# Kernel optimization log

Measured on AMD Instinct MI355X. Metric: run time of the kernel, lower is better.

Reference implementation:

```python
import jax, jax.numpy as jnp
import numpy as np

B, T, M, D = 2, 2048, 2048, 128
H = M // D
ROTARY_BASE = 10000
NORM_EPS = 1e-6
QK_SCALE = 1.0 / D  # mult = sqrt(qk_scale) applied to both q and k
INFTY_APPROX = 1e30


def setup_inputs() -> dict:
    key = jax.random.key(0)
    ks = jax.random.split(key, 6)
    w_scale = M ** (-0.5)
    return {
        "x": jax.random.normal(ks[0], (B, T, M), jnp.float32),
        "wq": jax.random.normal(ks[1], (M, H, D), jnp.float32) * w_scale,
        "wk": jax.random.normal(ks[2], (M, H, D), jnp.float32) * w_scale,
        "wv": jax.random.normal(ks[3], (M, H, D), jnp.float32) * w_scale,
        "wo": jax.random.normal(ks[4], (H, D, M), jnp.float32) * w_scale,
        "gq": jnp.zeros((H, 1, D), jnp.float32),
        "bq": jnp.zeros((H, 1, D), jnp.float32),
        "gk": jnp.zeros((H, 1, D), jnp.float32),
        "bk": jnp.zeros((H, 1, D), jnp.float32),
    }


def _qk_layernorm(x, g, b):
    # x: [B,H,T,D]; g,b: [H,1,D]; centered RMS norm with trainable (1+g), b
    x = x - jnp.mean(x, axis=-1, keepdims=True)
    x = x / jnp.sqrt(jnp.mean(jnp.square(x), axis=-1, keepdims=True) + NORM_EPS)
    return x * (1.0 + g)[None] + b[None]


def _rotary(x):
    # x: [B,H,T,D]; half-split rotary encoding
    half = D // 2
    positions = jnp.arange(T, dtype=jnp.float32)[:, None]          # [T,1]
    ang_freqs = jnp.power(float(ROTARY_BASE), -jnp.arange(half, dtype=jnp.float32) / half)[None, :]  # [1,half]
    radians = positions * ang_freqs                                  # [T,half]
    cos = jnp.cos(radians)[None, None].astype(x.dtype)               # [1,1,T,half]
    sin = jnp.sin(radians)[None, None].astype(x.dtype)
    even, odd = jnp.split(x, 2, axis=-1)
    return jnp.concatenate([even * cos - odd * sin, even * sin + odd * cos], axis=-1)


def reference(x, wq, wk, wv, wo, gq, bq, gk, bk):
    q = jnp.einsum('bim,mhd->bhid', x, wq)
    k = jnp.einsum('bim,mhd->bhid', x, wk)
    v = jnp.einsum('bim,mhd->bhid', x, wv)
    q = _rotary(_qk_layernorm(q, gq, bq))
    k = _rotary(_qk_layernorm(k, gk, bk))
    mult = jnp.asarray(QK_SCALE ** 0.5, dtype=x.dtype)
    s = jnp.einsum('bhid,bhjd->bhij', q * mult, k * mult)            # [B,H,T,T]
    i = jnp.arange(T)[:, None]
    j = jnp.arange(T)[None, :]
    future = (i < j)[None, None]                                      # mask future positions
    s = s - jnp.asarray(INFTY_APPROX, dtype=s.dtype) * future
    p = jax.nn.softmax(s, axis=-1)
    o = jnp.einsum('bhij,bhjd->bhid', p, v)
    return jnp.einsum('bhid,hdm->bim', o, wo)
```

## Files before the change

kernel.cpp:

```cpp
#include <hip/hip_runtime.h>


#define NB 2
#define NT 2048
#define NM 2048
#define NH 16
#define ND 128

typedef __attribute__((ext_vector_type(4))) float f32x4;
typedef __attribute__((ext_vector_type(8))) short bf16x8;
typedef __attribute__((ext_vector_type(4))) short bf16x4;

#define AS1 __attribute__((address_space(1)))
#define AS3 __attribute__((address_space(3)))

#define SW(r) (((r) ^ ((r) >> 2)) & 3)

__device__ __forceinline__ unsigned short f2bf(float f){
  unsigned int u = __float_as_uint(f);
  u = (u + 0x7fffu + ((u >> 16) & 1u)) >> 16;
  return (unsigned short)u;
}
__device__ __forceinline__ float bf2f(short s){
  return __uint_as_float(((unsigned int)(unsigned short)s) << 16);
}
__device__ __forceinline__ void gload_lds16(const void* g, void* l){
  __builtin_amdgcn_global_load_lds((const AS1 void*)g, (AS3 void*)l, 16, 0, 0);
}

__global__ __launch_bounds__(256) void prep_k(const float* __restrict__ x,
                                              const float* __restrict__ wq,
                                              const float* __restrict__ wk,
                                              const float* __restrict__ wv,
                                              const float* __restrict__ wo,
                                              short* __restrict__ xb,
                                              short* __restrict__ wT,
                                              float* __restrict__ ctab,
                                              float* __restrict__ stab){
  __shared__ float tl[32][33];
  const int bid = blockIdx.x, tid = threadIdx.x;
  if (bid < 8192){
    size_t gid = (size_t)bid * 256 + tid;
    float4 v = *(const float4*)(x + gid * 4);
    bf16x4 o;
    o[0] = (short)f2bf(v.x); o[1] = (short)f2bf(v.y);
    o[2] = (short)f2bf(v.z); o[3] = (short)f2bf(v.w);
    *(bf16x4*)(xb + gid * 4) = o;
  } else if (bid < 24576){
    int tb = bid - 8192;
    int z = tb >> 12, rem = tb & 4095;
    int n0 = (rem & 63) * 32, k0 = (rem >> 6) * 32;
    const float* src = (z == 0) ? wq : (z == 1) ? wk : (z == 2) ? wv : wo;
    short* dst = wT + (size_t)z * 2048 * 2048;
    int cx = tid & 31, ry = tid >> 5;
    #pragma unroll
    for (int p = 0; p < 4; ++p)
      tl[ry + 8 * p][cx] = src[(size_t)(k0 + ry + 8 * p) * 2048 + n0 + cx];
    __syncthreads();
    #pragma unroll
    for (int p = 0; p < 4; ++p){
      int n = n0 + ry + 8 * p;
      if (z < 2){
        int d = n & 127;
        n = (n & ~127) | (((d & 63) << 1) | (d >> 6));
      }
      dst[(size_t)n * 2048 + k0 + cx] = (short)f2bf(tl[cx][ry + 8 * p]);
    }
  } else {
    int t = (bid - 24576) * 4 + (tid >> 6);
    int i = tid & 63;
    float freq = __expf(-(float)i * (9.210340371976184f / 64.0f));
    float ang = (float)t * freq;
    ctab[t * 64 + i] = cosf(ang);
    stab[t * 64 + i] = sinf(ang);
  }
}

#define NKT2 64
__global__ __launch_bounds__(512, 4) void gemm256_k(const short* __restrict__ A,
                                                    const short* __restrict__ Bt,
                                                    short* __restrict__ Cv,
                                                    short* __restrict__ Cn,
                                                    const float* __restrict__ gq,
                                                    const float* __restrict__ bq,
                                                    const float* __restrict__ gk,
                                                    const float* __restrict__ bk,
                                                    const float* __restrict__ ctab,
                                                    const float* __restrict__ stab){
  extern __shared__ char lds[];
  const int tid = threadIdx.x;
  const int wid = tid >> 6, lane = tid & 63;
  const int lrow = lane & 15, g8 = lane >> 4;
  const int wm = wid >> 1, wn = wid & 1;
  const int Kdim = 2048;

  int bid = blockIdx.x;
  int s = (bid & 7) * 96 + (bid >> 3);
  const int bx = s & 15;
  const int by = s >> 4;
  const int m0 = bx * 256, n0 = by * 128;

  const int ar = lane >> 2;
  const int ag = (lane & 3) ^ SW(ar);
  const short* Ab = A  + (size_t)(m0 + wid * 32 + ar) * Kdim + ag * 8;
  const short* Bb = Bt + (size_t)(n0 + wid * 16 + ar) * Kdim + ag * 8;

  f32x4 acc[4][4] = {};

  auto STAGE = [&](int c, int kt){
    #pragma unroll
    for (int i = 0; i < 2; ++i)
      gload_lds16(Ab + (size_t)(i * 16) * Kdim + kt * 32,
                  lds + c * 16384 + wid * 2048 + i * 1024);
    gload_lds16(Bb + kt * 32, lds + 32768 + c * 8192 + wid * 1024);
  };
  auto ldA = [&](int c, int mi) -> bf16x8 {
    int row = wm * 64 + mi * 16 + lrow;
    return *(const bf16x8*)(lds + c * 16384 + row * 64 + ((g8 ^ SW(row)) << 4));
  };
  auto ldB = [&](int c, int ni) -> bf16x8 {
    int row = wn * 64 + ni * 16 + lrow;
    return *(const bf16x8*)(lds + 32768 + c * 8192 + row * 64 + ((g8 ^ SW(row)) << 4));
  };

  STAGE(0, 0);

  for (int kt = 0; kt < NKT2; ++kt){
    const int c = kt & 1;
    asm volatile("s_waitcnt vmcnt(0)" ::: "memory");
    __builtin_amdgcn_s_barrier();
    if (kt + 1 < NKT2) STAGE(c ^ 1, kt + 1);

    bf16x8 af[4], bfv[4];
    #pragma unroll
    for (int mi = 0; mi < 4; ++mi) af[mi] = ldA(c, mi);
    #pragma unroll
    for (int ni = 0; ni < 4; ++ni) bfv[ni] = ldB(c, ni);
    #pragma unroll
    for (int mi = 0; mi < 4; ++mi)
      #pragma unroll
      for (int ni = 0; ni < 4; ++ni)
        acc[mi][ni] = __builtin_amdgcn_mfma_f32_16x16x32_bf16(
            af[mi], bfv[ni], acc[mi][ni], 0, 0, 0);
  }

  const int tsel = by >> 4;
  const int hh = by & 15;
  if (tsel < 2){
    const float* gv = tsel ? gk : gq;
    const float* bv = tsel ? bk : bq;
    float* red = (float*)lds;
    float gcoef[4], bcoef[4];
    #pragma unroll
    for (int ni = 0; ni < 4; ++ni){
      int p = wn * 64 + ni * 16 + lrow;
      int d = (p >> 1) + ((p & 1) << 6);
      gcoef[ni] = 1.0f + gv[hh * 128 + d];
      bcoef[ni] = bv[hh * 128 + d];
    }
    __syncthreads();
    #pragma unroll
    for (int mi = 0; mi < 4; ++mi)
      #pragma unroll
      for (int r = 0; r < 4; ++r){
        float a0 = acc[mi][0][r], a1 = acc[mi][1][r];
        float a2 = acc[mi][2][r], a3 = acc[mi][3][r];
        float s1 = (a0 + a1) + (a2 + a3);
        float s2 = (a0*a0 + a1*a1) + (a2*a2 + a3*a3);
        #pragma unroll
        for (int off = 1; off < 16; off <<= 1){
          s1 += __shfl_xor(s1, off);
          s2 += __shfl_xor(s2, off);
        }
        if (lrow == 0){
          int row = wm * 64 + mi * 16 + g8 * 4 + r;
          red[row * 4 + wn * 2]     = s1;
          red[row * 4 + wn * 2 + 1] = s2;
        }
      }
    __syncthreads();
    const float qsc = tsel ? 1.0f : 0.011271055007f;
    const float sgn = (lrow & 1) ? 1.0f : -1.0f;
    short* dstn = Cn + (size_t)tsel * (NB * NH * NT * ND);
    #pragma unroll
    for (int mi = 0; mi < 4; ++mi)
      #pragma unroll
      for (int r = 0; r < 4; ++r){
        int row = wm * 64 + mi * 16 + g8 * 4 + r;
        float s1 = red[row * 4] + red[row * 4 + 2];
        float s2 = red[row * 4 + 1] + red[row * 4 + 3];
        float mean = s1 * (1.0f / 128.0f);
        float var = s2 * (1.0f / 128.0f) - mean * mean;
        float rstd = rsqrtf(var + 1e-6f);
        int rowb = m0 + row;
        int b = rowb >> 11, t = rowb & 2047;
        size_t rbase = (((size_t)(b * NH + hh)) * NT + t) * ND;
        #pragma unroll
        for (int ni = 0; ni < 4; ++ni){
          float nv = (acc[mi][ni][r] - mean) * rstd * gcoef[ni] + bcoef[ni];
          float pv = __shfl_xor(nv, 1);
          int p = wn * 64 + ni * 16 + lrow;
          float c = ctab[t * 64 + (p >> 1)], sn = stab[t * 64 + (p >> 1)];
          float o = (nv * c + sgn * pv * sn) * qsc;
          dstn[rbase + p] = (short)f2bf(o);
        }
      }
  } else {
    #pragma unroll
    for (int mi = 0; mi < 4; ++mi){
      int rowb = m0 + wm * 64 + mi * 16 + g8 * 4;
      int b = rowb >> 11, t0 = rowb & 2047;
      int jb = t0 >> 6, toff = t0 & 63;
      #pragma unroll
      for (int ni = 0; ni < 4; ++ni){
        int d = wn * 64 + ni * 16 + lrow;
        f32x4 a = acc[mi][ni];
        bf16x4 w4;
        #pragma unroll
        for (int r = 0; r < 4; ++r) w4[r] = (short)f2bf(a[r]);
        *(bf16x4*)&Cv[(((size_t)(b * NH + hh) * 32 + jb) * ND + d) * 64 + toff] = w4;
      }
    }
  }
}

__global__ __launch_bounds__(512, 4) void gemmo_k(const short* __restrict__ A,
                                                  const short* __restrict__ Bt,
                                                  float* __restrict__ Cout){
  extern __shared__ char lds[];
  const int tid = threadIdx.x;
  const int wid = tid >> 6, lane = tid & 63;
  const int lrow = lane & 15, g8 = lane >> 4;
  const int wm = wid >> 1, wn = wid & 1;
  const int Kdim = 2048;

  int bid = blockIdx.x;
  int s = (bid & 7) * 32 + (bid >> 3);
  const int bx = s & 15;
  const int by = s >> 4;
  const int m0 = bx * 256, n0 = by * 128;

  const int ar = lane >> 2;
  const int ag = (lane & 3) ^ SW(ar);
  const short* Ab = A  + (size_t)(m0 + wid * 32 + ar) * Kdim + ag * 8;
  const short* Bb = Bt + (size_t)(n0 + wid * 16 + ar) * Kdim + ag * 8;

  f32x4 acc[4][4] = {};

  auto STAGE = [&](int c, int kt){
    #pragma unroll
    for (int i = 0; i < 2; ++i)
      gload_lds16(Ab + (size_t)(i * 16) * Kdim + kt * 32,
                  lds + c * 16384 + wid * 2048 + i * 1024);
    gload_lds16(Bb + kt * 32, lds + 32768 + c * 8192 + wid * 1024);
  };
  auto ldA = [&](int c, int mi) -> bf16x8 {
    int row = wm * 64 + mi * 16 + lrow;
    return *(const bf16x8*)(lds + c * 16384 + row * 64 + ((g8 ^ SW(row)) << 4));
  };
  auto ldB = [&](int c, int ni) -> bf16x8 {
    int row = wn * 64 + ni * 16 + lrow;
    return *(const bf16x8*)(lds + 32768 + c * 8192 + row * 64 + ((g8 ^ SW(row)) << 4));
  };

  STAGE(0, 0);

  for (int kt = 0; kt < NKT2; ++kt){
    const int c = kt & 1;
    asm volatile("s_waitcnt vmcnt(0)" ::: "memory");
    __builtin_amdgcn_s_barrier();
    if (kt + 1 < NKT2) STAGE(c ^ 1, kt + 1);

    bf16x8 af[4], bfv[4];
    #pragma unroll
    for (int mi = 0; mi < 4; ++mi) af[mi] = ldA(c, mi);
    #pragma unroll
    for (int ni = 0; ni < 4; ++ni) bfv[ni] = ldB(c, ni);
    #pragma unroll
    for (int mi = 0; mi < 4; ++mi)
      #pragma unroll
      for (int ni = 0; ni < 4; ++ni)
        acc[mi][ni] = __builtin_amdgcn_mfma_f32_16x16x32_bf16(
            af[mi], bfv[ni], acc[mi][ni], 0, 0, 0);
  }

  #pragma unroll
  for (int mi = 0; mi < 4; ++mi){
    int rowb = m0 + wm * 64 + mi * 16 + g8 * 4;
    #pragma unroll
    for (int ni = 0; ni < 4; ++ni){
      int col = n0 + wn * 64 + ni * 16 + lrow;
      f32x4 a = acc[mi][ni];
      #pragma unroll
      for (int r = 0; r < 4; ++r)
        Cout[(size_t)(rowb + r) * 2048 + col] = a[r];
    }
  }
}

__global__ __launch_bounds__(512) void attn_k(const short* __restrict__ qn,
                                              const short* __restrict__ kn,
                                              const short* __restrict__ vt,
                                              short* __restrict__ ob){
  extern __shared__ char lds[];
  const int tid = threadIdx.x;
  const int wid = tid >> 6, lane = tid & 63;
  const int lrow = lane & 15, g8 = lane >> 4;
  const int id = blockIdx.x;
  const int qs = id >> 5;
  const int bh = id & 31;
  const int b = bh >> 4, h = bh & 15;
  const size_t base = (size_t)bh * NT * ND;
  char* Pw = lds + 98304 + wid * 2048;

  auto STAGE = [&](int jb){
    const int cb = jb % 3;
    #pragma unroll
    for (int i = 0; i < 2; ++i){
      int r0 = wid * 4 + i * 32;
      int r = r0 + (lane >> 4);
      int g = lane & 15;
      gload_lds16(kn + base + (size_t)(jb * 64 + r) * ND + ((g ^ (r & 7)) << 3),
                  lds + cb * 16384 + r0 * 256);
    }
    #pragma unroll
    for (int i = 0; i < 2; ++i){
      int d0 = wid * 8 + i * 64;
      int d = d0 + (lane >> 3);
      int g = lane & 7;
      gload_lds16(vt + base + (size_t)jb * 8192 + d * 64 + ((g ^ (d & 7)) << 3),
                  lds + 49152 + cb * 16384 + d0 * 128);
    }
  };

  for (int pass = 0; pass < 2; ++pass){
    const int qt = pass ? (15 - qs) : qs;
    const int t0 = qt * 128;
    const int wrow0 = t0 + wid * 16;
    const int tq = wrow0 + lrow;
    bf16x8 qf[4];
    #pragma unroll
    for (int dc = 0; dc < 4; ++dc)
      qf[dc] = *(const bf16x8*)(qn + base + (size_t)tq * ND + dc * 32 + g8 * 8);
    f32x4 O[8] = {};
    float m = -3e38f, lsum = 0.0f;
    const int ntiles = 2 * qt + 2;

    __syncthreads();
    STAGE(0);
    STAGE(1);

    for (int jb = 0; jb < ntiles; ++jb){
      if (jb + 1 < ntiles) asm volatile("s_waitcnt vmcnt(4)" ::: "memory");
      else                 asm volatile("s_waitcnt vmcnt(0)" ::: "memory");
      __builtin_amdgcn_s_barrier();
      if (jb + 2 < ntiles) STAGE(jb + 2);
      const char* Kb = lds + (jb % 3) * 16384;
      const char* Vb = lds + 49152 + (jb % 3) * 16384;

      if (jb * 64 <= wrow0 + 15){
        f32x4 st[4] = {};
        __builtin_amdgcn_s_setprio(1);
        #pragma unroll
        for (int dc = 0; dc < 4; ++dc)
          #pragma unroll
          for (int js = 0; js < 4; ++js){
            int jl = js * 16 + lrow;
            bf16x8 kf = *(const bf16x8*)(Kb + jl * 256 +
                          (((dc * 4 + g8) ^ (jl & 7)) << 4));
            st[js] = __builtin_amdgcn_mfma_f32_16x16x32_bf16(kf, qf[dc], st[js], 0, 0, 0);
          }
        __builtin_amdgcn_s_setprio(0);
        if (jb * 64 + 63 > wrow0){
          #pragma unroll
          for (int js = 0; js < 4; ++js)
            #pragma unroll
            for (int r = 0; r < 4; ++r){
              int j = jb * 64 + js * 16 + g8 * 4 + r;
              if (j > tq) st[js][r] = -3e38f;
            }
        }
        f32x4 m4 = st[0];
        #pragma unroll
        for (int js = 1; js < 4; ++js)
          #pragma unroll
          for (int r = 0; r < 4; ++r) m4[r] = fmaxf(m4[r], st[js][r]);
        float mx = fmaxf(fmaxf(m4[0], m4[1]), fmaxf(m4[2], m4[3]));
        mx = fmaxf(mx, __shfl_xor(mx, 16));
        mx = fmaxf(mx, __shfl_xor(mx, 32));
        if (!__all(mx <= m + 8.0f)){
          float mnew = fmaxf(m, mx);
          float fac = exp2f(m - mnew);
          m = mnew;
          lsum *= fac;
          #pragma unroll
          for (int dcb = 0; dcb < 8; ++dcb) O[dcb] *= fac;
        }
        float ps = 0.0f;
        #pragma unroll
        for (int js = 0; js < 4; ++js){
          float p0 = exp2f(st[js][0] - m);
          float p1 = exp2f(st[js][1] - m);
          float p2 = exp2f(st[js][2] - m);
          float p3 = exp2f(st[js][3] - m);
          ps += (p0 + p1) + (p2 + p3);
          unsigned int lo, hi;
          asm("v_cvt_pk_bf16_f32 %0, %1, %2" : "=v"(lo) : "v"(p0), "v"(p1));
          asm("v_cvt_pk_bf16_f32 %0, %1, %2" : "=v"(hi) : "v"(p2), "v"(p3));
          uint2 w; w.x = lo; w.y = hi;
          *(uint2*)(Pw + lrow * 128 + ((js * 32 + g8 * 8) ^ ((lrow & 7) << 4))) = w;
        }
        ps += __shfl_xor(ps, 16);
        ps += __shfl_xor(ps, 32);
        lsum += ps;
        asm volatile("s_waitcnt lgkmcnt(0)" ::: "memory");
        __builtin_amdgcn_s_setprio(1);
        #pragma unroll
        for (int j32 = 0; j32 < 2; ++j32){
          bf16x8 pf = *(const bf16x8*)(Pw + lrow * 128 +
                        ((j32 * 64 + g8 * 16) ^ ((lrow & 7) << 4)));
          #pragma unroll
          for (int dcb = 0; dcb < 8; ++dcb){
            int d = dcb * 16 + lrow;
            bf16x8 vf = *(const bf16x8*)(Vb + d * 128 +
                          (((j32 * 4 + g8) ^ (d & 7)) << 4));
            O[dcb] = __builtin_amdgcn_mfma_f32_16x16x32_bf16(vf, pf, O[dcb], 0, 0, 0);
          }
        }
        __builtin_amdgcn_s_setprio(0);
      }
    }
    float inv = 1.0f / lsum;
    #pragma unroll
    for (int dcb = 0; dcb < 8; ++dcb){
      bf16x4 w4;
      #pragma unroll
      for (int r = 0; r < 4; ++r) w4[r] = (short)f2bf(O[dcb][r] * inv);
      *(bf16x4*)(ob + ((size_t)(b * NT + tq)) * (NH * ND) + h * ND + dcb * 16 + g8 * 4) = w4;
    }
  }
}

extern "C" void kernel_launch(void* const* d_in, const int* in_sizes, int n_in,
                              void* d_out, int out_size, void* d_ws, size_t ws_size,
                              hipStream_t stream){
  const float* x  = (const float*)d_in[0];
  const float* wq = (const float*)d_in[1];
  const float* wk = (const float*)d_in[2];
  const float* wv = (const float*)d_in[3];
  const float* wo = (const float*)d_in[4];
  const float* gq = (const float*)d_in[5];
  const float* bq = (const float*)d_in[6];
  const float* gk = (const float*)d_in[7];
  const float* bk = (const float*)d_in[8];

  char* ws = (char*)d_ws;
  short* xb   = (short*)(ws);
  short* wT   = (short*)(ws + 16777216);
  short* qkvb = (short*)(ws + 50331648);
  short* qkn  = (short*)(ws + 100663296);
  short* ob   = (short*)(ws + 134217728);
  float* ctab = (float*)(ws + 150994944);
  float* stab = (float*)(ws + 151519232);

  (void)hipFuncSetAttribute((const void*)gemm256_k,
                            hipFuncAttributeMaxDynamicSharedMemorySize, 49152);
  (void)hipFuncSetAttribute((const void*)gemmo_k,
                            hipFuncAttributeMaxDynamicSharedMemorySize, 49152);
  (void)hipFuncSetAttribute((const void*)attn_k,
                            hipFuncAttributeMaxDynamicSharedMemorySize, 114688);

  prep_k<<<dim3(25088), dim3(256), 0, stream>>>(x, wq, wk, wv, wo, xb, wT, ctab, stab);
  gemm256_k<<<dim3(768), dim3(512), 49152, stream>>>(xb, wT,
                                                     qkvb + 2 * (size_t)8388608, qkn,
                                                     gq, bq, gk, bk, ctab, stab);
  attn_k<<<dim3(256), dim3(512), 114688, stream>>>(qkn, qkn + 8388608,
                                                   qkvb + 2 * (size_t)8388608, ob);
  gemmo_k<<<dim3(256), dim3(512), 49152, stream>>>(ob, wT + 3 * (size_t)4194304,
                                                   (float*)d_out);
}
```

Baseline: 258.9 us.

## Restructure projection GEMMs to 128x256 tiles with 4 waves

Both projection GEMMs change from 512-thread blocks with 256x128 tiles to 256-thread blocks with 128x256 tiles. Each wave now computes a 128x64 subtile with 8x4 MFMA accumulators, so it reads more A fragments from LDS per B fragment. The QK-norm reduction is reworked so each block covers two heads, with per-head partial sums kept in LDS. This doubles accumulator registers per wave and halves the waves per block, which may lower occupancy and the ability to hide latency.

```diff
diff --git a/kernel.cpp b/kernel.cpp
--- a/kernel.cpp
+++ b/kernel.cpp
@@ -77,7 +77,7 @@
 }
 
 #define NKT2 64
-__global__ __launch_bounds__(512, 4) void gemm256_k(const short* __restrict__ A,
+__global__ __launch_bounds__(256, 2) void gemm256_k(const short* __restrict__ A,
                                                     const short* __restrict__ Bt,
                                                     short* __restrict__ Cv,
                                                     short* __restrict__ Cn,
@@ -91,36 +91,38 @@
   const int tid = threadIdx.x;
   const int wid = tid >> 6, lane = tid & 63;
   const int lrow = lane & 15, g8 = lane >> 4;
-  const int wm = wid >> 1, wn = wid & 1;
   const int Kdim = 2048;
 
   int bid = blockIdx.x;
   int s = (bid & 7) * 96 + (bid >> 3);
-  const int bx = s & 15;
-  const int by = s >> 4;
-  const int m0 = bx * 256, n0 = by * 128;
+  const int bx = s & 31;
+  const int by = s >> 5;
+  const int m0 = bx * 128, n0 = by * 256;
 
   const int ar = lane >> 2;
   const int ag = (lane & 3) ^ SW(ar);
   const short* Ab = A  + (size_t)(m0 + wid * 32 + ar) * Kdim + ag * 8;
-  const short* Bb = Bt + (size_t)(n0 + wid * 16 + ar) * Kdim + ag * 8;
-
-  f32x4 acc[4][4] = {};
+  const short* Bb = Bt + (size_t)(n0 + wid * 64 + ar) * Kdim + ag * 8;
+
+  f32x4 acc[8][4] = {};
 
   auto STAGE = [&](int c, int kt){
     #pragma unroll
     for (int i = 0; i < 2; ++i)
       gload_lds16(Ab + (size_t)(i * 16) * Kdim + kt * 32,
-                  lds + c * 16384 + wid * 2048 + i * 1024);
-    gload_lds16(Bb + kt * 32, lds + 32768 + c * 8192 + wid * 1024);
+                  lds + c * 8192 + wid * 2048 + i * 1024);
+    #pragma unroll
+    for (int j = 0; j < 4; ++j)
+      gload_lds16(Bb + (size_t)(j * 16) * Kdim + kt * 32,
+                  lds + 16384 + c * 16384 + wid * 4096 + j * 1024);
   };
   auto ldA = [&](int c, int mi) -> bf16x8 {
-    int row = wm * 64 + mi * 16 + lrow;
-    return *(const bf16x8*)(lds + c * 16384 + row * 64 + ((g8 ^ SW(row)) << 4));
+    int row = mi * 16 + lrow;
+    return *(const bf16x8*)(lds + c * 8192 + row * 64 + ((g8 ^ SW(row)) << 4));
   };
   auto ldB = [&](int c, int ni) -> bf16x8 {
-    int row = wn * 64 + ni * 16 + lrow;
-    return *(const bf16x8*)(lds + 32768 + c * 8192 + row * 64 + ((g8 ^ SW(row)) << 4));
+    int row = wid * 64 + ni * 16 + lrow;
+    return *(const bf16x8*)(lds + 16384 + c * 16384 + row * 64 + ((g8 ^ SW(row)) << 4));
   };
 
   STAGE(0, 0);
@@ -131,21 +133,22 @@
     __builtin_amdgcn_s_barrier();
     if (kt + 1 < NKT2) STAGE(c ^ 1, kt + 1);
 
-    bf16x8 af[4], bfv[4];
-    #pragma unroll
-    for (int mi = 0; mi < 4; ++mi) af[mi] = ldA(c, mi);
+    bf16x8 af[8], bfv[4];
+    #pragma unroll
+    for (int mi = 0; mi < 8; ++mi) af[mi] = ldA(c, mi);
     #pragma unroll
     for (int ni = 0; ni < 4; ++ni) bfv[ni] = ldB(c, ni);
     #pragma unroll
-    for (int mi = 0; mi < 4; ++mi)
+    for (int mi = 0; mi < 8; ++mi)
       #pragma unroll
       for (int ni = 0; ni < 4; ++ni)
         acc[mi][ni] = __builtin_amdgcn_mfma_f32_16x16x32_bf16(
             af[mi], bfv[ni], acc[mi][ni], 0, 0, 0);
   }
 
-  const int tsel = by >> 4;
-  const int hh = by & 15;
+  const int tsel = by >> 3;
+  const int hcol = wid >> 1;
+  const int hh = (by & 7) * 2 + hcol;
   if (tsel < 2){
     const float* gv = tsel ? gk : gq;
     const float* bv = tsel ? bk : bq;
@@ -153,14 +156,14 @@
     float gcoef[4], bcoef[4];
     #pragma unroll
     for (int ni = 0; ni < 4; ++ni){
-      int p = wn * 64 + ni * 16 + lrow;
+      int p = (wid & 1) * 64 + ni * 16 + lrow;
       int d = (p >> 1) + ((p & 1) << 6);
       gcoef[ni] = 1.0f + gv[hh * 128 + d];
       bcoef[ni] = bv[hh * 128 + d];
     }
     __syncthreads();
     #pragma unroll
-    for (int mi = 0; mi < 4; ++mi)
+    for (int mi = 0; mi < 8; ++mi)
       #pragma unroll
       for (int r = 0; r < 4; ++r){
         float a0 = acc[mi][0][r], a1 = acc[mi][1][r];
@@ -173,9 +176,9 @@
           s2 += __shfl_xor(s2, off);
         }
         if (lrow == 0){
-          int row = wm * 64 + mi * 16 + g8 * 4 + r;
-          red[row * 4 + wn * 2]     = s1;
-          red[row * 4 + wn * 2 + 1] = s2;
+          int row = mi * 16 + g8 * 4 + r;
+          red[row * 8 + hcol * 4 + (wid & 1) * 2]     = s1;
+          red[row * 8 + hcol * 4 + (wid & 1) * 2 + 1] = s2;
         }
       }
     __syncthreads();
@@ -183,12 +186,12 @@
     const float sgn = (lrow & 1) ? 1.0f : -1.0f;
     short* dstn = Cn + (size_t)tsel * (NB * NH * NT * ND);
     #pragma unroll
-    for (int mi = 0; mi < 4; ++mi)
+    for (int mi = 0; mi < 8; ++mi)
       #pragma unroll
       for (int r = 0; r < 4; ++r){
-        int row = wm * 64 + mi * 16 + g8 * 4 + r;
-        float s1 = red[row * 4] + red[row * 4 + 2];
-        float s2 = red[row * 4 + 1] + red[row * 4 + 3];
+        int row = mi * 16 + g8 * 4 + r;
+        float s1 = red[row * 8 + hcol * 4]     + red[row * 8 + hcol * 4 + 2];
+        float s2 = red[row * 8 + hcol * 4 + 1] + red[row * 8 + hcol * 4 + 3];
         float mean = s1 * (1.0f / 128.0f);
         float var = s2 * (1.0f / 128.0f) - mean * mean;
         float rstd = rsqrtf(var + 1e-6f);
@@ -199,7 +202,7 @@
         for (int ni = 0; ni < 4; ++ni){
           float nv = (acc[mi][ni][r] - mean) * rstd * gcoef[ni] + bcoef[ni];
           float pv = __shfl_xor(nv, 1);
-          int p = wn * 64 + ni * 16 + lrow;
+          int p = (wid & 1) * 64 + ni * 16 + lrow;
           float c = ctab[t * 64 + (p >> 1)], sn = stab[t * 64 + (p >> 1)];
           float o = (nv * c + sgn * pv * sn) * qsc;
           dstn[rbase + p] = (short)f2bf(o);
@@ -207,13 +210,13 @@
       }
   } else {
     #pragma unroll
-    for (int mi = 0; mi < 4; ++mi){
-      int rowb = m0 + wm * 64 + mi * 16 + g8 * 4;
+    for (int mi = 0; mi < 8; ++mi){
+      int rowb = m0 + mi * 16 + g8 * 4;
       int b = rowb >> 11, t0 = rowb & 2047;
       int jb = t0 >> 6, toff = t0 & 63;
       #pragma unroll
       for (int ni = 0; ni < 4; ++ni){
-        int d = wn * 64 + ni * 16 + lrow;
+        int d = (wid & 1) * 64 + ni * 16 + lrow;
         f32x4 a = acc[mi][ni];
         bf16x4 w4;
         #pragma unroll
@@ -224,43 +227,45 @@
   }
 }
 
-__global__ __launch_bounds__(512, 4) void gemmo_k(const short* __restrict__ A,
+__global__ __launch_bounds__(256, 2) void gemmo_k(const short* __restrict__ A,
                                                   const short* __restrict__ Bt,
                                                   float* __restrict__ Cout){
   extern __shared__ char lds[];
   const int tid = threadIdx.x;
   const int wid = tid >> 6, lane = tid & 63;
   const int lrow = lane & 15, g8 = lane >> 4;
-  const int wm = wid >> 1, wn = wid & 1;
   const int Kdim = 2048;
 
   int bid = blockIdx.x;
   int s = (bid & 7) * 32 + (bid >> 3);
-  const int bx = s & 15;
-  const int by = s >> 4;
-  const int m0 = bx * 256, n0 = by * 128;
+  const int bx = s & 31;
+  const int by = s >> 5;
+  const int m0 = bx * 128, n0 = by * 256;
 
   const int ar = lane >> 2;
   const int ag = (lane & 3) ^ SW(ar);
   const short* Ab = A  + (size_t)(m0 + wid * 32 + ar) * Kdim + ag * 8;
-  const short* Bb = Bt + (size_t)(n0 + wid * 16 + ar) * Kdim + ag * 8;
-
-  f32x4 acc[4][4] = {};
+  const short* Bb = Bt + (size_t)(n0 + wid * 64 + ar) * Kdim + ag * 8;
+
+  f32x4 acc[8][4] = {};
 
   auto STAGE = [&](int c, int kt){
     #pragma unroll
     for (int i = 0; i < 2; ++i)
       gload_lds16(Ab + (size_t)(i * 16) * Kdim + kt * 32,
-                  lds + c * 16384 + wid * 2048 + i * 1024);
-    gload_lds16(Bb + kt * 32, lds + 32768 + c * 8192 + wid * 1024);
+                  lds + c * 8192 + wid * 2048 + i * 1024);
+    #pragma unroll
+    for (int j = 0; j < 4; ++j)
+      gload_lds16(Bb + (size_t)(j * 16) * Kdim + kt * 32,
+                  lds + 16384 + c * 16384 + wid * 4096 + j * 1024);
   };
   auto ldA = [&](int c, int mi) -> bf16x8 {
-    int row = wm * 64 + mi * 16 + lrow;
-    return *(const bf16x8*)(lds + c * 16384 + row * 64 + ((g8 ^ SW(row)) << 4));
+    int row = mi * 16 + lrow;
+    return *(const bf16x8*)(lds + c * 8192 + row * 64 + ((g8 ^ SW(row)) << 4));
   };
   auto ldB = [&](int c, int ni) -> bf16x8 {
-    int row = wn * 64 + ni * 16 + lrow;
-    return *(const bf16x8*)(lds + 32768 + c * 8192 + row * 64 + ((g8 ^ SW(row)) << 4));
+    int row = wid * 64 + ni * 16 + lrow;
+    return *(const bf16x8*)(lds + 16384 + c * 16384 + row * 64 + ((g8 ^ SW(row)) << 4));
   };
 
   STAGE(0, 0);
@@ -271,13 +276,13 @@
     __builtin_amdgcn_s_barrier();
     if (kt + 1 < NKT2) STAGE(c ^ 1, kt + 1);
 
-    bf16x8 af[4], bfv[4];
-    #pragma unroll
-    for (int mi = 0; mi < 4; ++mi) af[mi] = ldA(c, mi);
+    bf16x8 af[8], bfv[4];
+    #pragma unroll
+    for (int mi = 0; mi < 8; ++mi) af[mi] = ldA(c, mi);
     #pragma unroll
     for (int ni = 0; ni < 4; ++ni) bfv[ni] = ldB(c, ni);
     #pragma unroll
-    for (int mi = 0; mi < 4; ++mi)
+    for (int mi = 0; mi < 8; ++mi)
       #pragma unroll
       for (int ni = 0; ni < 4; ++ni)
         acc[mi][ni] = __builtin_amdgcn_mfma_f32_16x16x32_bf16(
@@ -285,11 +290,11 @@
   }
 
   #pragma unroll
-  for (int mi = 0; mi < 4; ++mi){
-    int rowb = m0 + wm * 64 + mi * 16 + g8 * 4;
+  for (int mi = 0; mi < 8; ++mi){
+    int rowb = m0 + mi * 16 + g8 * 4;
     #pragma unroll
     for (int ni = 0; ni < 4; ++ni){
-      int col = n0 + wn * 64 + ni * 16 + lrow;
+      int col = n0 + wid * 64 + ni * 16 + lrow;
       f32x4 a = acc[mi][ni];
       #pragma unroll
       for (int r = 0; r < 4; ++r)
@@ -471,11 +476,11 @@
                             hipFuncAttributeMaxDynamicSharedMemorySize, 114688);
 
   prep_k<<<dim3(25088), dim3(256), 0, stream>>>(x, wq, wk, wv, wo, xb, wT, ctab, stab);
-  gemm256_k<<<dim3(768), dim3(512), 49152, stream>>>(xb, wT,
+  gemm256_k<<<dim3(768), dim3(256), 49152, stream>>>(xb, wT,
                                                      qkvb + 2 * (size_t)8388608, qkn,
                                                      gq, bq, gk, bk, ctab, stab);
   attn_k<<<dim3(256), dim3(512), 114688, stream>>>(qkn, qkn + 8388608,
                                                    qkvb + 2 * (size_t)8388608, ob);
-  gemmo_k<<<dim3(256), dim3(512), 49152, stream>>>(ob, wT + 3 * (size_t)4194304,
+  gemmo_k<<<dim3(256), dim3(256), 49152, stream>>>(ob, wT + 3 * (size_t)4194304,
                                                    (float*)d_out);
 }
```

Result: slower. 285.5 us (+10.3%).
